# Kernel optimization log

Hardware: AMD Instinct MI355X
Metric: run time of the kernel (lower is better)

## Reference

```python
import jax, jax.numpy as jnp
import numpy as np

N_NODES = 100000
N_EDGES = 3200000
IN_DIM = 11
HID = 32


def setup_inputs() -> dict:
    key = jax.random.key(0)
    ks = jax.random.split(key, 12)
    inp = {
        "x": jax.random.normal(ks[0], (N_NODES, IN_DIM), dtype=jnp.float32),
        "edge_index": jax.random.randint(ks[1], (2, N_EDGES), 0, N_NODES, dtype=jnp.int32),
        "batch": jnp.zeros((N_NODES,), dtype=jnp.int32),
        # GCNConv layer 1 (11 -> 32)
        "W1": jax.random.normal(ks[2], (IN_DIM, HID), dtype=jnp.float32) / np.sqrt(IN_DIM),
        "b1": jnp.zeros((HID,), dtype=jnp.float32),
        # GCNConv layer 2 (32 -> 32)
        "W2": jax.random.normal(ks[3], (HID, HID), dtype=jnp.float32) / np.sqrt(HID),
        "b2": jnp.zeros((HID,), dtype=jnp.float32),
        # output MLP: 32 -> 16 -> 1
        "Wo1": jax.random.normal(ks[4], (HID, HID // 2), dtype=jnp.float32) / np.sqrt(HID),
        "bo1": jnp.zeros((HID // 2,), dtype=jnp.float32),
        "Wo2": jax.random.normal(ks[5], (HID // 2, 1), dtype=jnp.float32) / np.sqrt(HID // 2),
        "bo2": jnp.zeros((1,), dtype=jnp.float32),
    }
    return inp


def _gcn_norm(edge_index, n_nodes):
    # Add self-loops and compute symmetric normalization (PyG GCNConv default).
    loops = jnp.arange(n_nodes, dtype=edge_index.dtype)
    src = jnp.concatenate([edge_index[0], loops])
    dst = jnp.concatenate([edge_index[1], loops])
    ones = jnp.ones_like(dst, dtype=jnp.float32)
    deg = jax.ops.segment_sum(ones, dst, num_segments=n_nodes)  # degree of A+I on target side
    dinv = jax.lax.rsqrt(deg)  # deg >= 1 thanks to self-loops
    norm = dinv[src] * dinv[dst]  # [E+N]
    return src, dst, norm


def _gcn_conv(x, W, b, src, dst, norm, n_nodes):
    xw = x @ W                                   # transform first (small dim)
    msg = norm[:, None] * xw[src]                # gather + scale  [E+N, H]
    agg = jax.ops.segment_sum(msg, dst, num_segments=n_nodes)  # scatter-add
    return agg + b


def reference(x, edge_index, batch, W1, b1, W2, b2, Wo1, bo1, Wo2, bo2):
    n = x.shape[0]
    src, dst, norm = _gcn_norm(edge_index, n)
    h = jax.nn.relu(_gcn_conv(x, W1, b1, src, dst, norm, n))
    # F.dropout(training=self.training) is identity in eval mode
    h = jax.nn.relu(_gcn_conv(h, W2, b2, src, dst, norm, n))
    h = jax.nn.elu(h @ Wo1 + bo1)
    out = h @ Wo2 + bo2
    return out.squeeze(-1)  # [N]
```

## Files before the change

kernel.cpp:

```cpp
#include <hip/hip_runtime.h>
#include <hip/hip_fp16.h>
#include <math.h>

#define N_NODES 100000
#define N_EDGES 3200000
#define IN_DIM 11
#define HID 32
#define HID2 16
#define SCHUNK 100352
#define BINSHIFT 8
#define BINSZ 256
#define NB 391
#define CHUNK 8192

__global__ __launch_bounds__(1024) void k_hist(const int* __restrict__ ei,
                                               int* __restrict__ bincnt) {
    __shared__ int h[NB];
    for (int i = threadIdx.x; i < NB; i += 1024) h[i] = 0;
    __syncthreads();
    int b0 = blockIdx.x * CHUNK;
    int e1 = b0 + CHUNK; if (e1 > N_EDGES) e1 = N_EDGES;
    for (int e = b0 + threadIdx.x; e < e1; e += 1024)
        atomicAdd(&h[ei[N_EDGES + e] >> BINSHIFT], 1);
    __syncthreads();
    for (int i = threadIdx.x; i < NB; i += 1024)
        if (h[i]) atomicAdd(&bincnt[i], h[i]);
}

__global__ __launch_bounds__(1024) void k_binscatter(const int* __restrict__ ei,
                                                     const int* __restrict__ bincnt,
                                                     int* __restrict__ bincur,
                                                     unsigned* __restrict__ binbuf) {
    __shared__ int pre[NB];
    __shared__ int h[NB];
    __shared__ int base[NB];
    __shared__ int tmp[512];
    int tid = threadIdx.x;
    int v = (tid < NB) ? bincnt[tid] : 0;
    if (tid < 512) tmp[tid] = v;
    __syncthreads();
    for (int off = 1; off < 512; off <<= 1) {
        int t = (tid < 512 && tid >= off) ? tmp[tid - off] : 0;
        __syncthreads();
        if (tid < 512) tmp[tid] += t;
        __syncthreads();
    }
    if (tid < NB) pre[tid] = tmp[tid] - v;
    for (int i = tid; i < NB; i += 1024) h[i] = 0;
    __syncthreads();
    int b0 = blockIdx.x * CHUNK;
    int e1 = b0 + CHUNK; if (e1 > N_EDGES) e1 = N_EDGES;
    for (int e = b0 + tid; e < e1; e += 1024)
        atomicAdd(&h[ei[N_EDGES + e] >> BINSHIFT], 1);
    __syncthreads();
    for (int i = tid; i < NB; i += 1024) {
        int c = h[i];
        if (c) base[i] = pre[i] + atomicAdd(&bincur[i], c);
        h[i] = 0;
    }
    __syncthreads();
    for (int e = b0 + tid; e < e1; e += 1024) {
        int d = ei[N_EDGES + e];
        int s = ei[e];
        int b = d >> BINSHIFT;
        int p = base[b] + atomicAdd(&h[b], 1);
        binbuf[p] = (unsigned)s | ((unsigned)(d & (BINSZ - 1)) << 17);
    }
}

__global__ __launch_bounds__(1024) void k_binfill(const unsigned* __restrict__ binbuf,
                                                  const int* __restrict__ bincnt,
                                                  int* __restrict__ rowstart,
                                                  float* __restrict__ dinv,
                                                  int* __restrict__ csr_src) {
    int b = blockIdx.x;
    int tid = threadIdx.x;
    __shared__ int tmp[512];
    __shared__ int cnt[BINSZ];
    __shared__ int rloc[BINSZ];
    __shared__ int cur[BINSZ];
    int v = (tid < 512 && tid < b) ? bincnt[tid] : 0;
    if (tid < 512) tmp[tid] = v;
    __syncthreads();
    for (int off = 256; off >= 1; off >>= 1) {
        if (tid < off) tmp[tid] += tmp[tid + off];
        __syncthreads();
    }
    int ebeg = tmp[0];
    int eend = ebeg + bincnt[b];
    __syncthreads();
    if (tid < BINSZ) cnt[tid] = 0;
    __syncthreads();
    for (int e = ebeg + tid; e < eend; e += 1024)
        atomicAdd(&cnt[binbuf[e] >> 17], 1);
    __syncthreads();
    int c = (tid < BINSZ) ? cnt[tid] : 0;
    if (tid < BINSZ) tmp[tid] = c;
    __syncthreads();
    for (int off = 1; off < BINSZ; off <<= 1) {
        int t = (tid < BINSZ && tid >= off) ? tmp[tid - off] : 0;
        __syncthreads();
        if (tid < BINSZ) tmp[tid] += t;
        __syncthreads();
    }
    if (tid < BINSZ) {
        rloc[tid] = tmp[tid] - c;
        cur[tid] = 0;
        int node = b * BINSZ + tid;
        if (node < N_NODES) {
            rowstart[node] = ebeg + rloc[tid];
            dinv[node] = rsqrtf((float)c + 1.0f);
        }
    }
    if (b == 0 && tid == 0) rowstart[N_NODES] = N_EDGES;
    __syncthreads();
    for (int e = ebeg + tid; e < eend; e += 1024) {
        unsigned vv = binbuf[e];
        int dl = vv >> 17;
        int s = (int)(vv & 0x1FFFFu);
        int p = ebeg + rloc[dl] + atomicAdd(&cur[dl], 1);
        csr_src[p] = s;
    }
}

__global__ void k_xw1(const float* __restrict__ x, const float* __restrict__ W1,
                      const float* __restrict__ dinv, __half* __restrict__ xwh) {
    int t = blockIdx.x * blockDim.x + threadIdx.x;
    int node = t >> 5;
    int j = t & 31;
    __shared__ float sW[IN_DIM * HID];
    __shared__ float sx[8 * IN_DIM];
    for (int i = threadIdx.x; i < IN_DIM * HID; i += 256) sW[i] = W1[i];
    int base = blockIdx.x * 8;
    if (threadIdx.x < 8 * IN_DIM) sx[threadIdx.x] = x[base * IN_DIM + threadIdx.x];
    __syncthreads();
    int ln = node - base;
    float acc = 0.0f;
#pragma unroll
    for (int k = 0; k < IN_DIM; ++k)
        acc += sx[ln * IN_DIM + k] * sW[k * HID + j];
    xwh[t] = __float2half(dinv[node] * acc);
}

__global__ void k_xw2(const float* __restrict__ h, const float* __restrict__ W2,
                      const float* __restrict__ dinv, __half* __restrict__ xwh) {
    int t = blockIdx.x * blockDim.x + threadIdx.x;
    int node = t >> 5;
    int j = t & 31;
    __shared__ float sW[HID * HID];
    for (int i = threadIdx.x; i < HID * HID; i += 256) sW[i] = W2[i];
    __syncthreads();
    float acc = 0.0f;
#pragma unroll
    for (int k = 0; k < HID; ++k)
        acc += h[node * HID + k] * sW[k * HID + j];
    xwh[t] = __float2half(dinv[node] * acc);
}

__global__ __launch_bounds__(256) void k_gather(const int* __restrict__ rowstart,
                                                const float* __restrict__ dinv,
                                                const int* __restrict__ csr_src,
                                                const __half* __restrict__ xwh,
                                                const float* __restrict__ bias,
                                                float* __restrict__ outb) {
    int node = blockIdx.x * 8 + (threadIdx.x >> 5);
    int j = threadIdx.x & 31;
    int beg = rowstart[node];
    int end = rowstart[node + 1];
    float acc = 0.0f;
    int e = beg;
    for (; e + 8 <= end; e += 8) {
        int s0 = csr_src[e],     s1 = csr_src[e + 1], s2 = csr_src[e + 2], s3 = csr_src[e + 3];
        int s4 = csr_src[e + 4], s5 = csr_src[e + 5], s6 = csr_src[e + 6], s7 = csr_src[e + 7];
        float x0 = __half2float(xwh[s0 * HID + j]);
        float x1 = __half2float(xwh[s1 * HID + j]);
        float x2 = __half2float(xwh[s2 * HID + j]);
        float x3 = __half2float(xwh[s3 * HID + j]);
        float x4 = __half2float(xwh[s4 * HID + j]);
        float x5 = __half2float(xwh[s5 * HID + j]);
        float x6 = __half2float(xwh[s6 * HID + j]);
        float x7 = __half2float(xwh[s7 * HID + j]);
        acc += ((x0 + x1) + (x2 + x3)) + ((x4 + x5) + (x6 + x7));
    }
    for (; e + 2 <= end; e += 2) {
        int s0 = csr_src[e], s1 = csr_src[e + 1];
        acc += __half2float(xwh[s0 * HID + j]) + __half2float(xwh[s1 * HID + j]);
    }
    for (; e < end; ++e)
        acc += __half2float(xwh[csr_src[e] * HID + j]);
    float dd = dinv[node];
    float v = dd * (acc + __half2float(xwh[node * HID + j])) + bias[j];
    outb[node * HID + j] = v > 0.0f ? v : 0.0f;
}

__global__ __launch_bounds__(256) void k_gather_mlp(const int* __restrict__ rowstart,
                                                    const float* __restrict__ dinv,
                                                    const int* __restrict__ csr_src,
                                                    const __half* __restrict__ xwh,
                                                    const float* __restrict__ b2,
                                                    const float* __restrict__ Wo1,
                                                    const float* __restrict__ bo1,
                                                    const float* __restrict__ Wo2,
                                                    const float* __restrict__ bo2,
                                                    float* __restrict__ out) {
    __shared__ float sW1[HID * HID2];
    __shared__ float sb1[HID2];
    __shared__ float sW2[HID2];
    __shared__ float sb2[HID];
    __shared__ float sH[8 * 33];
    for (int i = threadIdx.x; i < HID * HID2; i += 256) sW1[i] = Wo1[i];
    if (threadIdx.x < HID2) {
        sb1[threadIdx.x] = bo1[threadIdx.x];
        sW2[threadIdx.x] = Wo2[threadIdx.x];
    }
    if (threadIdx.x < HID) sb2[threadIdx.x] = b2[threadIdx.x];

    int ln = threadIdx.x >> 5;
    int node = blockIdx.x * 8 + ln;
    int j = threadIdx.x & 31;
    int beg = rowstart[node];
    int end = rowstart[node + 1];
    float acc = 0.0f;
    int e = beg;
    for (; e + 8 <= end; e += 8) {
        int s0 = csr_src[e],     s1 = csr_src[e + 1], s2 = csr_src[e + 2], s3 = csr_src[e + 3];
        int s4 = csr_src[e + 4], s5 = csr_src[e + 5], s6 = csr_src[e + 6], s7 = csr_src[e + 7];
        float x0 = __half2float(xwh[s0 * HID + j]);
        float x1 = __half2float(xwh[s1 * HID + j]);
        float x2 = __half2float(xwh[s2 * HID + j]);
        float x3 = __half2float(xwh[s3 * HID + j]);
        float x4 = __half2float(xwh[s4 * HID + j]);
        float x5 = __half2float(xwh[s5 * HID + j]);
        float x6 = __half2float(xwh[s6 * HID + j]);
        float x7 = __half2float(xwh[s7 * HID + j]);
        acc += ((x0 + x1) + (x2 + x3)) + ((x4 + x5) + (x6 + x7));
    }
    for (; e + 2 <= end; e += 2) {
        int s0 = csr_src[e], s1 = csr_src[e + 1];
        acc += __half2float(xwh[s0 * HID + j]) + __half2float(xwh[s1 * HID + j]);
    }
    for (; e < end; ++e)
        acc += __half2float(xwh[csr_src[e] * HID + j]);
    float dd = dinv[node];
    float hv = dd * (acc + __half2float(xwh[node * HID + j])) + sb2[j];
    sH[ln * 33 + j] = hv > 0.0f ? hv : 0.0f;
    __syncthreads();

    float val = 0.0f;
    if (j < HID2) {
        float a = sb1[j];
#pragma unroll
        for (int k = 0; k < HID; ++k) a += sH[ln * 33 + k] * sW1[k * HID2 + j];
        a = a > 0.0f ? a : (expf(a) - 1.0f);
        val = a * sW2[j];
    }
#pragma unroll
    for (int d = 16; d >= 1; d >>= 1) val += __shfl_down(val, d, 32);
    if (j == 0) out[node] = val + bo2[0];
}

extern "C" void kernel_launch(void* const* d_in, const int* in_sizes, int n_in,
                              void* d_out, int out_size, void* d_ws, size_t ws_size,
                              hipStream_t stream) {
    const float* x   = (const float*)d_in[0];
    const int*   ei  = (const int*)d_in[1];
    const float* W1  = (const float*)d_in[3];
    const float* b1  = (const float*)d_in[4];
    const float* W2  = (const float*)d_in[5];
    const float* b2  = (const float*)d_in[6];
    const float* Wo1 = (const float*)d_in[7];
    const float* bo1 = (const float*)d_in[8];
    const float* Wo2 = (const float*)d_in[9];
    const float* bo2 = (const float*)d_in[10];
    float* out = (float*)d_out;

    int*   bincnt   = (int*)d_ws;
    int*   bincur   = bincnt + 512;
    int*   rowstart = bincur + 512;
    float* dinv     = (float*)(rowstart + SCHUNK);
    int*   csr_src  = (int*)(dinv + SCHUNK);
    float* H        = (float*)(csr_src + N_EDGES);
    __half* XWH     = (__half*)(H + (size_t)N_NODES * HID);
    unsigned* binbuf = (unsigned*)H;

    const int BT = 256;
    int gNH  = (N_NODES * HID + BT - 1) / BT;
    int gC   = (N_EDGES + CHUNK - 1) / CHUNK;
    int gG   = N_NODES / 8;

    hipMemsetAsync(bincnt, 0, 1024 * sizeof(int), stream);
    k_hist      <<<gC, 1024, 0, stream>>>(ei, bincnt);
    k_binscatter<<<gC, 1024, 0, stream>>>(ei, bincnt, bincur, binbuf);
    k_binfill   <<<NB, 1024, 0, stream>>>(binbuf, bincnt, rowstart, dinv, csr_src);

    k_xw1<<<gNH, BT, 0, stream>>>(x, W1, dinv, XWH);
    k_gather<<<gG, BT, 0, stream>>>(rowstart, dinv, csr_src, XWH, b1, H);

    k_xw2<<<gNH, BT, 0, stream>>>(H, W2, dinv, XWH);
    k_gather_mlp<<<gG, BT, 0, stream>>>(rowstart, dinv, csr_src, XWH,
                                        b2, Wo1, bo1, Wo2, bo2, out);
}
```

Measured before the change: 291.5 us.

## Fuse layer-1 gather with W2 transform and vectorize CSR index loads

```diff
diff --git a/kernel.cpp b/kernel.cpp
--- a/kernel.cpp
+++ b/kernel.cpp
@@ -142,55 +142,64 @@
     xwh[t] = __float2half(dinv[node] * acc);
 }
 
-__global__ void k_xw2(const float* __restrict__ h, const float* __restrict__ W2,
-                      const float* __restrict__ dinv, __half* __restrict__ xwh) {
-    int t = blockIdx.x * blockDim.x + threadIdx.x;
-    int node = t >> 5;
-    int j = t & 31;
-    __shared__ float sW[HID * HID];
-    for (int i = threadIdx.x; i < HID * HID; i += 256) sW[i] = W2[i];
-    __syncthreads();
-    float acc = 0.0f;
-#pragma unroll
-    for (int k = 0; k < HID; ++k)
-        acc += h[node * HID + k] * sW[k * HID + j];
-    xwh[t] = __float2half(dinv[node] * acc);
-}
-
-__global__ __launch_bounds__(256) void k_gather(const int* __restrict__ rowstart,
-                                                const float* __restrict__ dinv,
-                                                const int* __restrict__ csr_src,
-                                                const __half* __restrict__ xwh,
-                                                const float* __restrict__ bias,
-                                                float* __restrict__ outb) {
-    int node = blockIdx.x * 8 + (threadIdx.x >> 5);
-    int j = threadIdx.x & 31;
-    int beg = rowstart[node];
-    int end = rowstart[node + 1];
+__device__ __forceinline__ float edge_accum(int beg, int end, int j,
+                                            const int* __restrict__ csr_src,
+                                            const __half* __restrict__ xwh) {
     float acc = 0.0f;
     int e = beg;
+    while (e < end && (e & 3)) {
+        acc += __half2float(xwh[csr_src[e] * HID + j]);
+        ++e;
+    }
     for (; e + 8 <= end; e += 8) {
-        int s0 = csr_src[e],     s1 = csr_src[e + 1], s2 = csr_src[e + 2], s3 = csr_src[e + 3];
-        int s4 = csr_src[e + 4], s5 = csr_src[e + 5], s6 = csr_src[e + 6], s7 = csr_src[e + 7];
-        float x0 = __half2float(xwh[s0 * HID + j]);
-        float x1 = __half2float(xwh[s1 * HID + j]);
-        float x2 = __half2float(xwh[s2 * HID + j]);
-        float x3 = __half2float(xwh[s3 * HID + j]);
-        float x4 = __half2float(xwh[s4 * HID + j]);
-        float x5 = __half2float(xwh[s5 * HID + j]);
-        float x6 = __half2float(xwh[s6 * HID + j]);
-        float x7 = __half2float(xwh[s7 * HID + j]);
+        int4 i0 = *(const int4*)(csr_src + e);
+        int4 i1 = *(const int4*)(csr_src + e + 4);
+        float x0 = __half2float(xwh[i0.x * HID + j]);
+        float x1 = __half2float(xwh[i0.y * HID + j]);
+        float x2 = __half2float(xwh[i0.z * HID + j]);
+        float x3 = __half2float(xwh[i0.w * HID + j]);
+        float x4 = __half2float(xwh[i1.x * HID + j]);
+        float x5 = __half2float(xwh[i1.y * HID + j]);
+        float x6 = __half2float(xwh[i1.z * HID + j]);
+        float x7 = __half2float(xwh[i1.w * HID + j]);
         acc += ((x0 + x1) + (x2 + x3)) + ((x4 + x5) + (x6 + x7));
     }
-    for (; e + 2 <= end; e += 2) {
-        int s0 = csr_src[e], s1 = csr_src[e + 1];
-        acc += __half2float(xwh[s0 * HID + j]) + __half2float(xwh[s1 * HID + j]);
+    if (e + 4 <= end) {
+        int4 i0 = *(const int4*)(csr_src + e);
+        acc += (__half2float(xwh[i0.x * HID + j]) + __half2float(xwh[i0.y * HID + j])) +
+               (__half2float(xwh[i0.z * HID + j]) + __half2float(xwh[i0.w * HID + j]));
+        e += 4;
     }
     for (; e < end; ++e)
         acc += __half2float(xwh[csr_src[e] * HID + j]);
+    return acc;
+}
+
+__global__ __launch_bounds__(256) void k_gather_xw2(const int* __restrict__ rowstart,
+                                                    const float* __restrict__ dinv,
+                                                    const int* __restrict__ csr_src,
+                                                    const __half* __restrict__ xwh1,
+                                                    const float* __restrict__ b1,
+                                                    const float* __restrict__ W2,
+                                                    __half* __restrict__ xwh2) {
+    __shared__ float sW2[HID * HID];
+    __shared__ float sH[8 * 33];
+    for (int i = threadIdx.x; i < HID * HID; i += 256) sW2[i] = W2[i];
+    __syncthreads();
+
+    int ln = threadIdx.x >> 5;
+    int node = blockIdx.x * 8 + ln;
+    int j = threadIdx.x & 31;
+    float acc = edge_accum(rowstart[node], rowstart[node + 1], j, csr_src, xwh1);
     float dd = dinv[node];
-    float v = dd * (acc + __half2float(xwh[node * HID + j])) + bias[j];
-    outb[node * HID + j] = v > 0.0f ? v : 0.0f;
+    float hv = dd * (acc + __half2float(xwh1[node * HID + j])) + b1[j];
+    sH[ln * 33 + j] = hv > 0.0f ? hv : 0.0f;
+    __syncthreads();
+
+    float a2 = 0.0f;
+#pragma unroll
+    for (int k = 0; k < HID; ++k) a2 += sH[ln * 33 + k] * sW2[k * HID + j];
+    xwh2[node * HID + j] = __float2half(dd * a2);
 }
 
 __global__ __launch_bounds__(256) void k_gather_mlp(const int* __restrict__ rowstart,
@@ -214,33 +223,12 @@
         sW2[threadIdx.x] = Wo2[threadIdx.x];
     }
     if (threadIdx.x < HID) sb2[threadIdx.x] = b2[threadIdx.x];
+    __syncthreads();
 
     int ln = threadIdx.x >> 5;
     int node = blockIdx.x * 8 + ln;
     int j = threadIdx.x & 31;
-    int beg = rowstart[node];
-    int end = rowstart[node + 1];
-    float acc = 0.0f;
-    int e = beg;
-    for (; e + 8 <= end; e += 8) {
-        int s0 = csr_src[e],     s1 = csr_src[e + 1], s2 = csr_src[e + 2], s3 = csr_src[e + 3];
-        int s4 = csr_src[e + 4], s5 = csr_src[e + 5], s6 = csr_src[e + 6], s7 = csr_src[e + 7];
-        float x0 = __half2float(xwh[s0 * HID + j]);
-        float x1 = __half2float(xwh[s1 * HID + j]);
-        float x2 = __half2float(xwh[s2 * HID + j]);
-        float x3 = __half2float(xwh[s3 * HID + j]);
-        float x4 = __half2float(xwh[s4 * HID + j]);
-        float x5 = __half2float(xwh[s5 * HID + j]);
-        float x6 = __half2float(xwh[s6 * HID + j]);
-        float x7 = __half2float(xwh[s7 * HID + j]);
-        acc += ((x0 + x1) + (x2 + x3)) + ((x4 + x5) + (x6 + x7));
-    }
-    for (; e + 2 <= end; e += 2) {
-        int s0 = csr_src[e], s1 = csr_src[e + 1];
-        acc += __half2float(xwh[s0 * HID + j]) + __half2float(xwh[s1 * HID + j]);
-    }
-    for (; e < end; ++e)
-        acc += __half2float(xwh[csr_src[e] * HID + j]);
+    float acc = edge_accum(rowstart[node], rowstart[node + 1], j, csr_src, xwh);
     float dd = dinv[node];
     float hv = dd * (acc + __half2float(xwh[node * HID + j])) + sb2[j];
     sH[ln * 33 + j] = hv > 0.0f ? hv : 0.0f;
@@ -274,14 +262,14 @@
     const float* bo2 = (const float*)d_in[10];
     float* out = (float*)d_out;
 
-    int*   bincnt   = (int*)d_ws;
-    int*   bincur   = bincnt + 512;
-    int*   rowstart = bincur + 512;
-    float* dinv     = (float*)(rowstart + SCHUNK);
-    int*   csr_src  = (int*)(dinv + SCHUNK);
-    float* H        = (float*)(csr_src + N_EDGES);
-    __half* XWH     = (__half*)(H + (size_t)N_NODES * HID);
-    unsigned* binbuf = (unsigned*)H;
+    int*      bincnt   = (int*)d_ws;
+    int*      bincur   = bincnt + 512;
+    int*      rowstart = bincur + 512;
+    float*    dinv     = (float*)(rowstart + SCHUNK);
+    int*      csr_src  = (int*)(dinv + SCHUNK);
+    unsigned* binbuf   = (unsigned*)(csr_src + N_EDGES);
+    __half*   XWH1     = (__half*)(binbuf + N_EDGES);
+    __half*   XWH2     = XWH1 + (size_t)N_NODES * HID;
 
     const int BT = 256;
     int gNH  = (N_NODES * HID + BT - 1) / BT;
@@ -293,10 +281,9 @@
     k_binscatter<<<gC, 1024, 0, stream>>>(ei, bincnt, bincur, binbuf);
     k_binfill   <<<NB, 1024, 0, stream>>>(binbuf, bincnt, rowstart, dinv, csr_src);
 
-    k_xw1<<<gNH, BT, 0, stream>>>(x, W1, dinv, XWH);
-    k_gather<<<gG, BT, 0, stream>>>(rowstart, dinv, csr_src, XWH, b1, H);
-
-    k_xw2<<<gNH, BT, 0, stream>>>(H, W2, dinv, XWH);
-    k_gather_mlp<<<gG, BT, 0, stream>>>(rowstart, dinv, csr_src, XWH,
+    k_xw1<<<gNH, BT, 0, stream>>>(x, W1, dinv, XWH1);
+    k_gather_xw2<<<gG, BT, 0, stream>>>(rowstart, dinv, csr_src, XWH1, b1, W2, XWH2);
+
+    k_gather_mlp<<<gG, BT, 0, stream>>>(rowstart, dinv, csr_src, XWH2,
                                         b2, Wo1, bo1, Wo2, bo2, out);
 }
```

Result: no change. 291.6 us (+0.1%).
